# Kernel optimization log

Measured on AMD Instinct MI355X. Metric: run time of the kernel, lower is better.

The kernel has to match this reference:

```python
import jax, jax.numpy as jnp
import numpy as np

TAU = 1.0


def setup_inputs() -> dict:
    key = jax.random.key(0)
    k1, k2 = jax.random.split(key)
    z = jax.random.normal(k1, (131072, 64), dtype=jnp.float32)
    cluster_centers = jax.random.normal(k2, (512, 64), dtype=jnp.float32)
    return {"z": z, "cluster_centers": cluster_centers}


def reference(z, cluster_centers):
    # ||z - c||^2 = ||z||^2 + ||c||^2 - 2 z.c  (avoids the [B,K,D] broadcast tensor)
    z_sq = jnp.sum(z * z, axis=1, keepdims=True)              # [B, 1]
    c_sq = jnp.sum(cluster_centers * cluster_centers, axis=1)  # [K]
    cross = jnp.einsum('bd,kd->bk', z, cluster_centers)        # [B, K]
    dist_sq = z_sq + c_sq[None, :] - 2.0 * cross               # [B, K]
    q = jax.nn.softmax(-dist_sq / TAU, axis=1)                 # [B, K]
    loss = jnp.mean(jnp.sum(q * dist_sq, axis=1))
    return (q, loss)
```

## Files before the change

### kernel.cpp

```cpp
#include <hip/hip_runtime.h>

typedef short bf16x8 __attribute__((ext_vector_type(8)));
typedef float f32x4 __attribute__((ext_vector_type(4)));

#define K_CLUSTERS 512
#define DIM 64
#define ROWS_PER_BLOCK 64
#define NSUB 4
#define QPAD 520

__device__ __forceinline__ unsigned short f32_to_bf16_rne(float f) {
    unsigned int u = __float_as_uint(f);
    u += 0x7fffu + ((u >> 16) & 1u);
    return (unsigned short)(u >> 16);
}
__device__ __forceinline__ float bf16_bits_to_f32(unsigned short h) {
    return __uint_as_float(((unsigned int)h) << 16);
}

__global__ void prep_centers(const float* __restrict__ c,
                             short* __restrict__ c_hi, short* __restrict__ c_lo,
                             float* __restrict__ c_sq, float* __restrict__ loss_out) {
    if (blockIdx.x == 0 && threadIdx.x == 0) loss_out[0] = 0.0f;
    int idx = blockIdx.x * 256 + threadIdx.x;
    float v = c[idx];
    unsigned short h = f32_to_bf16_rne(v);
    float hf = bf16_bits_to_f32(h);
    unsigned short l = f32_to_bf16_rne(v - hf);
    c_hi[idx] = (short)h;
    c_lo[idx] = (short)l;
    float s = v * v;
    #pragma unroll
    for (int off = 1; off < 64; off <<= 1) s += __shfl_xor(s, off, 64);
    if ((threadIdx.x & 63) == 0) c_sq[idx >> 6] = s;
}

#define BARRIER() do {                                      \
    asm volatile("s_waitcnt lgkmcnt(0)" ::: "memory");      \
    __builtin_amdgcn_s_barrier();                           \
} while (0)

__global__ __launch_bounds__(512, 4)
void cluster_kernel(const float* __restrict__ z,
                    const short* __restrict__ c_hi,
                    const short* __restrict__ c_lo,
                    const float* __restrict__ c_sq,
                    float* __restrict__ q_out,
                    float* __restrict__ loss_out,
                    float inv_b) {
    __shared__ __align__(16) short a_hi_s[NSUB][16][72];
    __shared__ __align__(16) short a_lo_s[NSUB][16][72];
    __shared__ __align__(16) float q_s[16][QPAD];
    __shared__ __align__(16) float2 red_s[2][8][16];
    __shared__ float wloss_s[8];

    const int tid  = threadIdx.x;
    const int lane = tid & 63;
    const int wave = tid >> 6;
    const int m    = lane & 15;
    const int qd   = lane >> 4;
    const long rb  = (long)blockIdx.x * ROWS_PER_BLOCK;

    bf16x8 bh[4][2], bl[4][2];
    float csq[4];
    #pragma unroll
    for (int t = 0; t < 4; ++t) {
        const int col = wave * 64 + t * 16 + m;
        const long boff = (long)col * DIM + qd * 8;
        #pragma unroll
        for (int kg = 0; kg < 2; ++kg) {
            bh[t][kg] = *(const bf16x8*)(c_hi + boff + kg * 32);
            bl[t][kg] = *(const bf16x8*)(c_lo + boff + kg * 32);
        }
        csq[t] = c_sq[col];
    }

    const float2* zin = (const float2*)(z + rb * DIM);
    const int srow = tid >> 5;
    const int scol = (tid & 31) * 2;
    float zpart = 0.0f;
    #pragma unroll
    for (int k = 0; k < NSUB; ++k) {
        float2 v = zin[k * 512 + tid];
        zpart += v.x * v.x + v.y * v.y;
        unsigned short hx = f32_to_bf16_rne(v.x);
        unsigned short lx = f32_to_bf16_rne(v.x - bf16_bits_to_f32(hx));
        unsigned short hy = f32_to_bf16_rne(v.y);
        unsigned short ly = f32_to_bf16_rne(v.y - bf16_bits_to_f32(hy));
        *(unsigned int*)&a_hi_s[k][srow][scol] = (unsigned int)hx | ((unsigned int)hy << 16);
        *(unsigned int*)&a_lo_s[k][srow][scol] = (unsigned int)lx | ((unsigned int)ly << 16);
    }
    BARRIER();

    float lsum = 0.0f;

    for (int s = 0; s < NSUB; ++s) {
        bf16x8 ah[2], al[2];
        #pragma unroll
        for (int kg = 0; kg < 2; ++kg) {
            ah[kg] = *(const bf16x8*)&a_hi_s[s][m][kg * 32 + qd * 8];
            al[kg] = *(const bf16x8*)&a_lo_s[s][m][kg * 32 + qd * 8];
        }

        f32x4 acc[4];
        #pragma unroll
        for (int t = 0; t < 4; ++t) acc[t] = (f32x4){0.f, 0.f, 0.f, 0.f};
        #pragma unroll
        for (int kg = 0; kg < 2; ++kg) {
            #pragma unroll
            for (int t = 0; t < 4; ++t) {
                acc[t] = __builtin_amdgcn_mfma_f32_16x16x32_bf16(ah[kg], bh[t][kg], acc[t], 0, 0, 0);
                acc[t] = __builtin_amdgcn_mfma_f32_16x16x32_bf16(ah[kg], bl[t][kg], acc[t], 0, 0, 0);
                acc[t] = __builtin_amdgcn_mfma_f32_16x16x32_bf16(al[kg], bh[t][kg], acc[t], 0, 0, 0);
            }
        }

        float dd[4][4];
        #pragma unroll
        for (int t = 0; t < 4; ++t)
            #pragma unroll
            for (int r = 0; r < 4; ++r)
                dd[t][r] = __builtin_fmaf(-2.0f, acc[t][r], csq[t]);

        float mnw[4], sw4[4];
        #pragma unroll
        for (int r = 0; r < 4; ++r) {
            float mn0 = fminf(fminf(dd[0][r], dd[1][r]), fminf(dd[2][r], dd[3][r]));
            #pragma unroll
            for (int off = 1; off < 16; off <<= 1)
                mn0 = fminf(mn0, __shfl_xor(mn0, off, 64));
            mnw[r] = mn0;
        }
        #pragma unroll
        for (int r = 0; r < 4; ++r) {
            float s0 = (__expf(mnw[r] - dd[0][r]) + __expf(mnw[r] - dd[1][r]))
                     + (__expf(mnw[r] - dd[2][r]) + __expf(mnw[r] - dd[3][r]));
            #pragma unroll
            for (int off = 1; off < 16; off <<= 1)
                s0 += __shfl_xor(s0, off, 64);
            sw4[r] = s0;
        }
        if (m == 0) {
            #pragma unroll
            for (int r = 0; r < 4; ++r)
                red_s[s & 1][wave][qd * 4 + r] = make_float2(mnw[r], sw4[r]);
        }
        BARRIER();

        float mn = red_s[s & 1][0][m].x;
        #pragma unroll
        for (int w2 = 1; w2 < 8; ++w2) mn = fminf(mn, red_s[s & 1][w2][m].x);
        float S = 0.0f;
        #pragma unroll
        for (int w2 = 0; w2 < 8; ++w2) {
            float2 p = red_s[s & 1][w2][m];
            S = __builtin_fmaf(p.y, __expf(mn - p.x), S);
        }
        const float invS = 1.0f / S;

        float mnr[4], fsr[4];
        #pragma unroll
        for (int r = 0; r < 4; ++r) {
            mnr[r] = __shfl(mn,   qd * 4 + r, 64);
            fsr[r] = __shfl(invS, qd * 4 + r, 64);
        }

        #pragma unroll
        for (int r = 0; r < 4; ++r) {
            const int row = qd * 4 + r;
            #pragma unroll
            for (int t = 0; t < 4; ++t) {
                const float qv = __expf(mnr[r] - dd[t][r]) * fsr[r];
                q_s[row][wave * 64 + t * 16 + m] = qv;
                lsum = __builtin_fmaf(qv, dd[t][r], lsum);
            }
        }
        BARRIER();

        const long rbase = rb + (long)s * 16;
        #pragma unroll
        for (int rr = 0; rr < 2; ++rr) {
            const int row = wave * 2 + rr;
            const f32x4* src = (const f32x4*)&q_s[row][0];
            f32x4 v0 = src[lane];
            f32x4 v1 = src[64 + lane];
            f32x4* dst = (f32x4*)(q_out + (rbase + row) * K_CLUSTERS);
            dst[lane]      = v0;
            dst[64 + lane] = v1;
        }
    }

    float tot = lsum + zpart;
    #pragma unroll
    for (int off = 1; off < 64; off <<= 1) tot += __shfl_xor(tot, off, 64);
    if (lane == 0) wloss_s[wave] = tot;
    __syncthreads();
    if (tid == 0) {
        float t0 = 0.f;
        #pragma unroll
        for (int w = 0; w < 8; ++w) t0 += wloss_s[w];
        atomicAdd(loss_out, t0 * inv_b);
    }
}

extern "C" void kernel_launch(void* const* d_in, const int* in_sizes, int n_in,
                              void* d_out, int out_size, void* d_ws, size_t ws_size,
                              hipStream_t stream) {
    const float* z = (const float*)d_in[0];
    const float* c = (const float*)d_in[1];
    const int B = in_sizes[0] / DIM;
    float* q_out = (float*)d_out;
    float* loss_out = q_out + (size_t)B * K_CLUSTERS;

    char* ws = (char*)d_ws;
    short* c_hi = (short*)ws;
    short* c_lo = (short*)(ws + 65536);
    float* c_sq = (float*)(ws + 131072);

    prep_centers<<<(K_CLUSTERS * DIM) / 256, 256, 0, stream>>>(c, c_hi, c_lo, c_sq, loss_out);
    cluster_kernel<<<B / ROWS_PER_BLOCK, 512, 0, stream>>>(z, c_hi, c_lo, c_sq, q_out,
                                                           loss_out, 1.0f / (float)B);
}
```

Measured before the change: 337.5 us.

## Use persistent grid and fuse center preprocessing into main kernel

Replaces the one-block-per-64-rows launch (2048 blocks) with a persistent grid of 512 blocks that loop over row groups. Each block now loads fp32 centers directly, splitting them into hi/lo bf16 parts and computing their squared norms once, so the separate prep kernel and its workspace round trip go away. This is meant to cut per-block setup and launch overhead. In exchange each block does redundant center conversion, and the z load for the next group is no longer overlapped with other resident blocks' tails.

```diff
diff --git a/kernel.cpp b/kernel.cpp
--- a/kernel.cpp
+++ b/kernel.cpp
@@ -8,6 +8,7 @@
 #define ROWS_PER_BLOCK 64
 #define NSUB 4
 #define QPAD 520
+#define GRID 512
 
 __device__ __forceinline__ unsigned short f32_to_bf16_rne(float f) {
     unsigned int u = __float_as_uint(f);
@@ -18,21 +19,8 @@
     return __uint_as_float(((unsigned int)h) << 16);
 }
 
-__global__ void prep_centers(const float* __restrict__ c,
-                             short* __restrict__ c_hi, short* __restrict__ c_lo,
-                             float* __restrict__ c_sq, float* __restrict__ loss_out) {
-    if (blockIdx.x == 0 && threadIdx.x == 0) loss_out[0] = 0.0f;
-    int idx = blockIdx.x * 256 + threadIdx.x;
-    float v = c[idx];
-    unsigned short h = f32_to_bf16_rne(v);
-    float hf = bf16_bits_to_f32(h);
-    unsigned short l = f32_to_bf16_rne(v - hf);
-    c_hi[idx] = (short)h;
-    c_lo[idx] = (short)l;
-    float s = v * v;
-    #pragma unroll
-    for (int off = 1; off < 64; off <<= 1) s += __shfl_xor(s, off, 64);
-    if ((threadIdx.x & 63) == 0) c_sq[idx >> 6] = s;
+__global__ void zero_loss(float* __restrict__ loss_out) {
+    loss_out[0] = 0.0f;
 }
 
 #define BARRIER() do {                                      \
@@ -42,12 +30,10 @@
 
 __global__ __launch_bounds__(512, 4)
 void cluster_kernel(const float* __restrict__ z,
-                    const short* __restrict__ c_hi,
-                    const short* __restrict__ c_lo,
-                    const float* __restrict__ c_sq,
+                    const float* __restrict__ c,
                     float* __restrict__ q_out,
                     float* __restrict__ loss_out,
-                    float inv_b) {
+                    float inv_b, int totgroups) {
     __shared__ __align__(16) short a_hi_s[NSUB][16][72];
     __shared__ __align__(16) short a_lo_s[NSUB][16][72];
     __shared__ __align__(16) float q_s[16][QPAD];
@@ -59,134 +45,149 @@
     const int wave = tid >> 6;
     const int m    = lane & 15;
     const int qd   = lane >> 4;
-    const long rb  = (long)blockIdx.x * ROWS_PER_BLOCK;
+    const int srow = tid >> 5;
+    const int scol = (tid & 31) * 2;
 
     bf16x8 bh[4][2], bl[4][2];
     float csq[4];
     #pragma unroll
     for (int t = 0; t < 4; ++t) {
         const int col = wave * 64 + t * 16 + m;
-        const long boff = (long)col * DIM + qd * 8;
+        float part = 0.0f;
         #pragma unroll
         for (int kg = 0; kg < 2; ++kg) {
-            bh[t][kg] = *(const bf16x8*)(c_hi + boff + kg * 32);
-            bl[t][kg] = *(const bf16x8*)(c_lo + boff + kg * 32);
+            const float* cp = c + (long)col * DIM + kg * 32 + qd * 8;
+            bf16x8 h8, l8;
+            #pragma unroll
+            for (int j = 0; j < 8; ++j) {
+                const float v = cp[j];
+                part = __builtin_fmaf(v, v, part);
+                const unsigned short h = f32_to_bf16_rne(v);
+                h8[j] = (short)h;
+                l8[j] = (short)f32_to_bf16_rne(v - bf16_bits_to_f32(h));
+            }
+            bh[t][kg] = h8;
+            bl[t][kg] = l8;
         }
-        csq[t] = c_sq[col];
+        part += __shfl_xor(part, 16, 64);
+        part += __shfl_xor(part, 32, 64);
+        csq[t] = part;
     }
 
-    const float2* zin = (const float2*)(z + rb * DIM);
-    const int srow = tid >> 5;
-    const int scol = (tid & 31) * 2;
+    float lsum = 0.0f;
     float zpart = 0.0f;
-    #pragma unroll
-    for (int k = 0; k < NSUB; ++k) {
-        float2 v = zin[k * 512 + tid];
-        zpart += v.x * v.x + v.y * v.y;
-        unsigned short hx = f32_to_bf16_rne(v.x);
-        unsigned short lx = f32_to_bf16_rne(v.x - bf16_bits_to_f32(hx));
-        unsigned short hy = f32_to_bf16_rne(v.y);
-        unsigned short ly = f32_to_bf16_rne(v.y - bf16_bits_to_f32(hy));
-        *(unsigned int*)&a_hi_s[k][srow][scol] = (unsigned int)hx | ((unsigned int)hy << 16);
-        *(unsigned int*)&a_lo_s[k][srow][scol] = (unsigned int)lx | ((unsigned int)ly << 16);
-    }
-    BARRIER();
-
-    float lsum = 0.0f;
-
-    for (int s = 0; s < NSUB; ++s) {
-        bf16x8 ah[2], al[2];
+
+    for (int grp = blockIdx.x; grp < totgroups; grp += GRID) {
+        const long rb = (long)grp * ROWS_PER_BLOCK;
+        const float2* zin = (const float2*)(z + rb * DIM);
+
         #pragma unroll
-        for (int kg = 0; kg < 2; ++kg) {
-            ah[kg] = *(const bf16x8*)&a_hi_s[s][m][kg * 32 + qd * 8];
-            al[kg] = *(const bf16x8*)&a_lo_s[s][m][kg * 32 + qd * 8];
-        }
-
-        f32x4 acc[4];
-        #pragma unroll
-        for (int t = 0; t < 4; ++t) acc[t] = (f32x4){0.f, 0.f, 0.f, 0.f};
-        #pragma unroll
-        for (int kg = 0; kg < 2; ++kg) {
-            #pragma unroll
-            for (int t = 0; t < 4; ++t) {
-                acc[t] = __builtin_amdgcn_mfma_f32_16x16x32_bf16(ah[kg], bh[t][kg], acc[t], 0, 0, 0);
-                acc[t] = __builtin_amdgcn_mfma_f32_16x16x32_bf16(ah[kg], bl[t][kg], acc[t], 0, 0, 0);
-                acc[t] = __builtin_amdgcn_mfma_f32_16x16x32_bf16(al[kg], bh[t][kg], acc[t], 0, 0, 0);
-            }
-        }
-
-        float dd[4][4];
-        #pragma unroll
-        for (int t = 0; t < 4; ++t)
-            #pragma unroll
-            for (int r = 0; r < 4; ++r)
-                dd[t][r] = __builtin_fmaf(-2.0f, acc[t][r], csq[t]);
-
-        float mnw[4], sw4[4];
-        #pragma unroll
-        for (int r = 0; r < 4; ++r) {
-            float mn0 = fminf(fminf(dd[0][r], dd[1][r]), fminf(dd[2][r], dd[3][r]));
-            #pragma unroll
-            for (int off = 1; off < 16; off <<= 1)
-                mn0 = fminf(mn0, __shfl_xor(mn0, off, 64));
-            mnw[r] = mn0;
-        }
-        #pragma unroll
-        for (int r = 0; r < 4; ++r) {
-            float s0 = (__expf(mnw[r] - dd[0][r]) + __expf(mnw[r] - dd[1][r]))
-                     + (__expf(mnw[r] - dd[2][r]) + __expf(mnw[r] - dd[3][r]));
-            #pragma unroll
-            for (int off = 1; off < 16; off <<= 1)
-                s0 += __shfl_xor(s0, off, 64);
-            sw4[r] = s0;
-        }
-        if (m == 0) {
-            #pragma unroll
-            for (int r = 0; r < 4; ++r)
-                red_s[s & 1][wave][qd * 4 + r] = make_float2(mnw[r], sw4[r]);
+        for (int k = 0; k < NSUB; ++k) {
+            float2 v = zin[k * 512 + tid];
+            zpart += v.x * v.x + v.y * v.y;
+            unsigned short hx = f32_to_bf16_rne(v.x);
+            unsigned short lx = f32_to_bf16_rne(v.x - bf16_bits_to_f32(hx));
+            unsigned short hy = f32_to_bf16_rne(v.y);
+            unsigned short ly = f32_to_bf16_rne(v.y - bf16_bits_to_f32(hy));
+            *(unsigned int*)&a_hi_s[k][srow][scol] = (unsigned int)hx | ((unsigned int)hy << 16);
+            *(unsigned int*)&a_lo_s[k][srow][scol] = (unsigned int)lx | ((unsigned int)ly << 16);
         }
         BARRIER();
 
-        float mn = red_s[s & 1][0][m].x;
-        #pragma unroll
-        for (int w2 = 1; w2 < 8; ++w2) mn = fminf(mn, red_s[s & 1][w2][m].x);
-        float S = 0.0f;
-        #pragma unroll
-        for (int w2 = 0; w2 < 8; ++w2) {
-            float2 p = red_s[s & 1][w2][m];
-            S = __builtin_fmaf(p.y, __expf(mn - p.x), S);
-        }
-        const float invS = 1.0f / S;
-
-        float mnr[4], fsr[4];
-        #pragma unroll
-        for (int r = 0; r < 4; ++r) {
-            mnr[r] = __shfl(mn,   qd * 4 + r, 64);
-            fsr[r] = __shfl(invS, qd * 4 + r, 64);
-        }
-
-        #pragma unroll
-        for (int r = 0; r < 4; ++r) {
-            const int row = qd * 4 + r;
-            #pragma unroll
-            for (int t = 0; t < 4; ++t) {
-                const float qv = __expf(mnr[r] - dd[t][r]) * fsr[r];
-                q_s[row][wave * 64 + t * 16 + m] = qv;
-                lsum = __builtin_fmaf(qv, dd[t][r], lsum);
-            }
-        }
-        BARRIER();
-
-        const long rbase = rb + (long)s * 16;
-        #pragma unroll
-        for (int rr = 0; rr < 2; ++rr) {
-            const int row = wave * 2 + rr;
-            const f32x4* src = (const f32x4*)&q_s[row][0];
-            f32x4 v0 = src[lane];
-            f32x4 v1 = src[64 + lane];
-            f32x4* dst = (f32x4*)(q_out + (rbase + row) * K_CLUSTERS);
-            dst[lane]      = v0;
-            dst[64 + lane] = v1;
+        for (int s = 0; s < NSUB; ++s) {
+            bf16x8 ah[2], al[2];
+            #pragma unroll
+            for (int kg = 0; kg < 2; ++kg) {
+                ah[kg] = *(const bf16x8*)&a_hi_s[s][m][kg * 32 + qd * 8];
+                al[kg] = *(const bf16x8*)&a_lo_s[s][m][kg * 32 + qd * 8];
+            }
+
+            f32x4 acc[4];
+            #pragma unroll
+            for (int t = 0; t < 4; ++t) acc[t] = (f32x4){0.f, 0.f, 0.f, 0.f};
+            #pragma unroll
+            for (int kg = 0; kg < 2; ++kg) {
+                #pragma unroll
+                for (int t = 0; t < 4; ++t) {
+                    acc[t] = __builtin_amdgcn_mfma_f32_16x16x32_bf16(ah[kg], bh[t][kg], acc[t], 0, 0, 0);
+                    acc[t] = __builtin_amdgcn_mfma_f32_16x16x32_bf16(ah[kg], bl[t][kg], acc[t], 0, 0, 0);
+                    acc[t] = __builtin_amdgcn_mfma_f32_16x16x32_bf16(al[kg], bh[t][kg], acc[t], 0, 0, 0);
+                }
+            }
+
+            float dd[4][4];
+            #pragma unroll
+            for (int t = 0; t < 4; ++t)
+                #pragma unroll
+                for (int r = 0; r < 4; ++r)
+                    dd[t][r] = __builtin_fmaf(-2.0f, acc[t][r], csq[t]);
+
+            float mnw[4], sw4[4];
+            #pragma unroll
+            for (int r = 0; r < 4; ++r) {
+                float mn0 = fminf(fminf(dd[0][r], dd[1][r]), fminf(dd[2][r], dd[3][r]));
+                #pragma unroll
+                for (int off = 1; off < 16; off <<= 1)
+                    mn0 = fminf(mn0, __shfl_xor(mn0, off, 64));
+                mnw[r] = mn0;
+            }
+            #pragma unroll
+            for (int r = 0; r < 4; ++r) {
+                float s0 = (__expf(mnw[r] - dd[0][r]) + __expf(mnw[r] - dd[1][r]))
+                         + (__expf(mnw[r] - dd[2][r]) + __expf(mnw[r] - dd[3][r]));
+                #pragma unroll
+                for (int off = 1; off < 16; off <<= 1)
+                    s0 += __shfl_xor(s0, off, 64);
+                sw4[r] = s0;
+            }
+            if (m == 0) {
+                #pragma unroll
+                for (int r = 0; r < 4; ++r)
+                    red_s[s & 1][wave][qd * 4 + r] = make_float2(mnw[r], sw4[r]);
+            }
+            BARRIER();
+
+            float mn = red_s[s & 1][0][m].x;
+            #pragma unroll
+            for (int w2 = 1; w2 < 8; ++w2) mn = fminf(mn, red_s[s & 1][w2][m].x);
+            float S = 0.0f;
+            #pragma unroll
+            for (int w2 = 0; w2 < 8; ++w2) {
+                float2 p = red_s[s & 1][w2][m];
+                S = __builtin_fmaf(p.y, __expf(mn - p.x), S);
+            }
+            const float invS = 1.0f / S;
+
+            float mnr[4], fsr[4];
+            #pragma unroll
+            for (int r = 0; r < 4; ++r) {
+                mnr[r] = __shfl(mn,   qd * 4 + r, 64);
+                fsr[r] = __shfl(invS, qd * 4 + r, 64);
+            }
+
+            #pragma unroll
+            for (int r = 0; r < 4; ++r) {
+                const int row = qd * 4 + r;
+                #pragma unroll
+                for (int t = 0; t < 4; ++t) {
+                    const float qv = __expf(mnr[r] - dd[t][r]) * fsr[r];
+                    q_s[row][wave * 64 + t * 16 + m] = qv;
+                    lsum = __builtin_fmaf(qv, dd[t][r], lsum);
+                }
+            }
+            BARRIER();
+
+            const long rbase = rb + (long)s * 16;
+            #pragma unroll
+            for (int rr = 0; rr < 2; ++rr) {
+                const int row = wave * 2 + rr;
+                const f32x4* src = (const f32x4*)&q_s[row][0];
+                f32x4 v0 = src[lane];
+                f32x4 v1 = src[64 + lane];
+                f32x4* dst = (f32x4*)(q_out + (rbase + row) * K_CLUSTERS);
+                dst[lane]      = v0;
+                dst[64 + lane] = v1;
+            }
         }
     }
 
@@ -212,12 +213,10 @@
     float* q_out = (float*)d_out;
     float* loss_out = q_out + (size_t)B * K_CLUSTERS;
 
-    char* ws = (char*)d_ws;
-    short* c_hi = (short*)ws;
-    short* c_lo = (short*)(ws + 65536);
-    float* c_sq = (float*)(ws + 131072);
-
-    prep_centers<<<(K_CLUSTERS * DIM) / 256, 256, 0, stream>>>(c, c_hi, c_lo, c_sq, loss_out);
-    cluster_kernel<<<B / ROWS_PER_BLOCK, 512, 0, stream>>>(z, c_hi, c_lo, c_sq, q_out,
-                                                           loss_out, 1.0f / (float)B);
-}
+    zero_loss<<<1, 1, 0, stream>>>(loss_out);
+
+    const int totgroups = B / ROWS_PER_BLOCK;
+    const int grid = totgroups < GRID ? totgroups : GRID;
+    cluster_kernel<<<grid, 512, 0, stream>>>(z, c, q_out, loss_out,
+                                             1.0f / (float)B, totgroups);
+}
```

Result: slower. 354.6 us (+5.1%).

## Transpose MFMA operands so each lane owns a row and reuse exponentials

Applied to the files above, without the earlier changes.

Swaps the A/B operands of the MFMA so the accumulator layout gives each lane 4 consecutive cluster columns of one row. Per-row min and sum reductions then need only two cross-lane shuffles instead of four per row, and q can be written to shared memory as 16-byte vector stores. The exponentials from the partial softmax are kept and rescaled by one factor rather than recomputed, and the loss term comes from a single fused accumulation. The cost is more live registers for the stored exponentials, plus a QPAD change that alters shared-memory bank mapping for the new store pattern.

```diff
diff --git a/kernel.cpp b/kernel.cpp
--- a/kernel.cpp
+++ b/kernel.cpp
@@ -7,7 +7,7 @@
 #define DIM 64
 #define ROWS_PER_BLOCK 64
 #define NSUB 4
-#define QPAD 520
+#define QPAD 516
 
 __device__ __forceinline__ unsigned short f32_to_bf16_rne(float f) {
     unsigned int u = __float_as_uint(f);
@@ -59,10 +59,11 @@
     const int wave = tid >> 6;
     const int m    = lane & 15;
     const int qd   = lane >> 4;
+    const int srow = tid >> 5;
+    const int scol = (tid & 31) * 2;
     const long rb  = (long)blockIdx.x * ROWS_PER_BLOCK;
 
     bf16x8 bh[4][2], bl[4][2];
-    float csq[4];
     #pragma unroll
     for (int t = 0; t < 4; ++t) {
         const int col = wave * 64 + t * 16 + m;
@@ -72,12 +73,13 @@
             bh[t][kg] = *(const bf16x8*)(c_hi + boff + kg * 32);
             bl[t][kg] = *(const bf16x8*)(c_lo + boff + kg * 32);
         }
-        csq[t] = c_sq[col];
-    }
+    }
+    f32x4 csq4[4];
+    #pragma unroll
+    for (int t = 0; t < 4; ++t)
+        csq4[t] = *(const f32x4*)(c_sq + wave * 64 + t * 16 + qd * 4);
 
     const float2* zin = (const float2*)(z + rb * DIM);
-    const int srow = tid >> 5;
-    const int scol = (tid & 31) * 2;
     float zpart = 0.0f;
     #pragma unroll
     for (int k = 0; k < NSUB; ++k) {
@@ -109,9 +111,9 @@
         for (int kg = 0; kg < 2; ++kg) {
             #pragma unroll
             for (int t = 0; t < 4; ++t) {
-                acc[t] = __builtin_amdgcn_mfma_f32_16x16x32_bf16(ah[kg], bh[t][kg], acc[t], 0, 0, 0);
-                acc[t] = __builtin_amdgcn_mfma_f32_16x16x32_bf16(ah[kg], bl[t][kg], acc[t], 0, 0, 0);
-                acc[t] = __builtin_amdgcn_mfma_f32_16x16x32_bf16(al[kg], bh[t][kg], acc[t], 0, 0, 0);
+                acc[t] = __builtin_amdgcn_mfma_f32_16x16x32_bf16(bh[t][kg], ah[kg], acc[t], 0, 0, 0);
+                acc[t] = __builtin_amdgcn_mfma_f32_16x16x32_bf16(bl[t][kg], ah[kg], acc[t], 0, 0, 0);
+                acc[t] = __builtin_amdgcn_mfma_f32_16x16x32_bf16(bh[t][kg], al[kg], acc[t], 0, 0, 0);
             }
         }
 
@@ -120,31 +122,34 @@
         for (int t = 0; t < 4; ++t)
             #pragma unroll
             for (int r = 0; r < 4; ++r)
-                dd[t][r] = __builtin_fmaf(-2.0f, acc[t][r], csq[t]);
-
-        float mnw[4], sw4[4];
-        #pragma unroll
-        for (int r = 0; r < 4; ++r) {
-            float mn0 = fminf(fminf(dd[0][r], dd[1][r]), fminf(dd[2][r], dd[3][r]));
-            #pragma unroll
-            for (int off = 1; off < 16; off <<= 1)
-                mn0 = fminf(mn0, __shfl_xor(mn0, off, 64));
-            mnw[r] = mn0;
-        }
-        #pragma unroll
-        for (int r = 0; r < 4; ++r) {
-            float s0 = (__expf(mnw[r] - dd[0][r]) + __expf(mnw[r] - dd[1][r]))
-                     + (__expf(mnw[r] - dd[2][r]) + __expf(mnw[r] - dd[3][r]));
-            #pragma unroll
-            for (int off = 1; off < 16; off <<= 1)
-                s0 += __shfl_xor(s0, off, 64);
-            sw4[r] = s0;
-        }
-        if (m == 0) {
-            #pragma unroll
-            for (int r = 0; r < 4; ++r)
-                red_s[s & 1][wave][qd * 4 + r] = make_float2(mnw[r], sw4[r]);
-        }
+                dd[t][r] = __builtin_fmaf(-2.0f, acc[t][r], csq4[t][r]);
+
+        float mn0;
+        {
+            float a0 = fminf(fminf(dd[0][0], dd[0][1]), fminf(dd[0][2], dd[0][3]));
+            float a1 = fminf(fminf(dd[1][0], dd[1][1]), fminf(dd[1][2], dd[1][3]));
+            float a2 = fminf(fminf(dd[2][0], dd[2][1]), fminf(dd[2][2], dd[2][3]));
+            float a3 = fminf(fminf(dd[3][0], dd[3][1]), fminf(dd[3][2], dd[3][3]));
+            mn0 = fminf(fminf(a0, a1), fminf(a2, a3));
+        }
+        mn0 = fminf(mn0, __shfl_xor(mn0, 16, 64));
+        mn0 = fminf(mn0, __shfl_xor(mn0, 32, 64));
+        const float mnw = mn0;
+
+        float e[4][4], ssum = 0.0f, ped = 0.0f;
+        #pragma unroll
+        for (int t = 0; t < 4; ++t)
+            #pragma unroll
+            for (int r = 0; r < 4; ++r) {
+                e[t][r] = __expf(mnw - dd[t][r]);
+                ssum += e[t][r];
+                ped  = __builtin_fmaf(e[t][r], dd[t][r], ped);
+            }
+        ssum += __shfl_xor(ssum, 16, 64);
+        ssum += __shfl_xor(ssum, 32, 64);
+
+        if (qd == 0)
+            red_s[s & 1][wave][m] = make_float2(mnw, ssum);
         BARRIER();
 
         float mn = red_s[s & 1][0][m].x;
@@ -156,25 +161,16 @@
             float2 p = red_s[s & 1][w2][m];
             S = __builtin_fmaf(p.y, __expf(mn - p.x), S);
         }
-        const float invS = 1.0f / S;
-
-        float mnr[4], fsr[4];
-        #pragma unroll
-        for (int r = 0; r < 4; ++r) {
-            mnr[r] = __shfl(mn,   qd * 4 + r, 64);
-            fsr[r] = __shfl(invS, qd * 4 + r, 64);
-        }
-
-        #pragma unroll
-        for (int r = 0; r < 4; ++r) {
-            const int row = qd * 4 + r;
-            #pragma unroll
-            for (int t = 0; t < 4; ++t) {
-                const float qv = __expf(mnr[r] - dd[t][r]) * fsr[r];
-                q_s[row][wave * 64 + t * 16 + m] = qv;
-                lsum = __builtin_fmaf(qv, dd[t][r], lsum);
-            }
-        }
+        const float fac = __expf(mn - mnw) / S;
+
+        #pragma unroll
+        for (int t = 0; t < 4; ++t) {
+            f32x4 qv4;
+            #pragma unroll
+            for (int r = 0; r < 4; ++r) qv4[r] = e[t][r] * fac;
+            *(f32x4*)&q_s[m][wave * 64 + t * 16 + qd * 4] = qv4;
+        }
+        lsum = __builtin_fmaf(fac, ped, lsum);
         BARRIER();
 
         const long rbase = rb + (long)s * 16;
```

New measurement: 473.3 us. +40.2%, slower.
